# Kernel tuning notes

Measured on AMD Instinct MI355X. Metric: run time of the kernel, lower is better.

The kernel has to match this reference:

```python
import jax, jax.numpy as jnp
import numpy as np

S, N, L = 64, 256, 32
LANG_ID, D = 256, 128  # lang_od == pc_od == D
K = 16  # k; effective neighbors = k+1


def _mlp(x, w1, b1, w2, b2):
    return jnp.maximum(x @ w1 + b1, 0.0) @ w2 + b2


def setup_inputs() -> dict:
    key = jax.random.key(0)
    ks = jax.random.split(key, 16)
    def lin(k, fi, fo):
        return jax.random.normal(k, (fi, fo), jnp.float32) / np.sqrt(fi)
    inp = {
        "feat": jax.random.normal(ks[0], (S, N, D), jnp.float32),
        "coord": jax.random.normal(ks[1], (S, N, 3), jnp.float32),
        "lang_feat": jax.random.normal(ks[2], (S, L, LANG_ID), jnp.float32),
        "lang_len": jax.random.randint(ks[3], (S,), 1, L + 1),
        "rel_w1": lin(ks[4], 10, D), "rel_b1": jnp.zeros((D,), jnp.float32),
        "rel_w2": lin(ks[5], D, D), "rel_b2": jnp.zeros((D,), jnp.float32),
        "lang_w1": lin(ks[6], LANG_ID, D), "lang_b1": jnp.zeros((D,), jnp.float32),
        "lang_w2": lin(ks[7], D, D), "lang_b2": jnp.zeros((D,), jnp.float32),
        "feat_w1": lin(ks[8], D, D), "feat_b1": jnp.zeros((D,), jnp.float32),
        "feat_w2": lin(ks[9], D, D), "feat_b2": jnp.zeros((D,), jnp.float32),
    }
    return inp


def reference(feat, coord, lang_feat, lang_len,
              rel_w1, rel_b1, rel_w2, rel_b2,
              lang_w1, lang_b1, lang_w2, lang_b2,
              feat_w1, feat_b1, feat_w2, feat_b2):
    num_sen, num_obj, _ = feat.shape
    k1 = min(K, num_obj - 1) + 1  # k+1 neighbors including self
    # pairwise squared distances [S,N,N]
    d = ((coord[:, None, :, :] - coord[:, :, None, :]) ** 2).sum(-1)
    # k+1 nearest neighbors (smallest distance)
    _, idx = jax.lax.top_k(-d, k1)  # [S,N,k1]
    b = jnp.arange(num_sen)[:, None, None]
    coord_nb = coord[b, idx]  # [S,N,k1,3]
    coord_ctr = jnp.broadcast_to(coord[:, :, None, :], coord_nb.shape)
    rel_coord = coord_nb - coord_ctr
    dist = jnp.sqrt((rel_coord ** 2).sum(-1, keepdims=True))
    rel = jnp.concatenate([coord_nb, coord_ctr, rel_coord, dist], -1)  # [S,N,k1,10]
    rel = _mlp(rel, rel_w1, rel_b1, rel_w2, rel_b2)  # [S,N,k1,D]
    lang = _mlp(lang_feat, lang_w1, lang_b1, lang_w2, lang_b2)  # [S,L,D]
    f = _mlp(feat, feat_w1, feat_b1, feat_w2, feat_b2)  # [S,N,D]
    f_nb = f[b, idx]  # [S,N,k1,D]
    # attention of each (obj, neighbor) over language tokens
    attn = jnp.einsum('snkd,sld->snkl', f_nb, lang)
    attn = jax.nn.softmax(attn, axis=-1)
    max_len = lang_feat.shape[1]
    mask = (jnp.arange(max_len)[None, :] < lang_len[:, None]).astype(f.dtype)  # [S,L]
    attn = attn * mask[:, None, None, :]
    attn = attn / (attn.sum(-1, keepdims=True) + 1e-7)
    ins = jnp.einsum('snkl,sld->snkd', attn, lang)  # [S,N,k1,D]
    out = (f_nb * ins * rel).sum(2) + f  # [S,N,D]
    score = out.sum(-1)  # [S,N]
    return out, score
```

## Files before the change

### kernel.cpp

```cpp
#include <hip/hip_runtime.h>
#include <math.h>

#define S_ 64
#define N_ 256
#define L_ 32
#define D_ 128
#define LID_ 256
#define K1_ 17
#define CH_ 32
#define NW_ 8

typedef __attribute__((ext_vector_type(8))) short short8;
typedef __attribute__((ext_vector_type(4))) float f32x4;

__device__ __forceinline__ unsigned short f2bf(float f) {
  unsigned int u = __float_as_uint(f);
  u += 0x7fffu + ((u >> 16) & 1u);
  return (unsigned short)(u >> 16);
}


__global__ __launch_bounds__(256) void tar_prep_kernel(
    const float* __restrict__ rw1, const float* __restrict__ rb1,
    const float* __restrict__ rw2, const float* __restrict__ fw1,
    const float* __restrict__ fw2, unsigned short* __restrict__ w1T,
    unsigned short* __restrict__ w2T, unsigned short* __restrict__ fw1T,
    unsigned short* __restrict__ fw2T) {
  int t = blockIdx.x * 256 + threadIdx.x;
  int k = t >> 7, n = t & 127;
  int slot = 32 * (k >> 5) + 8 * ((k & 15) >> 2) + 4 * ((k >> 4) & 1) + (k & 3);
  w2T[(size_t)n * 128 + slot] = f2bf(rw2[(size_t)k * 128 + n]);
  fw1T[(size_t)n * 128 + k] = f2bf(fw1[(size_t)k * 128 + n]);
  fw2T[(size_t)n * 128 + k] = f2bf(fw2[(size_t)k * 128 + n]);
  if (t < 128 * 16) {
    int n2 = t >> 4, k2 = t & 15;
    unsigned short v = 0;
    if (k2 < 10) v = f2bf(rw1[(size_t)k2 * 128 + n2]);
    else if (k2 == 10) v = f2bf(rb1[n2]);
    w1T[(size_t)n2 * 16 + k2] = v;
  }
}

#define KNN_NB 1024
#define LANG_NB 1024
#define FM_NB 256
__global__ __launch_bounds__(256, 4) void tar_prologue(
    const float* __restrict__ coord, int* __restrict__ idx_out,
    const float* __restrict__ lx, const float* __restrict__ lw1,
    const float* __restrict__ lb1, const float* __restrict__ lw2,
    const float* __restrict__ lb2, unsigned short* __restrict__ lang_bf,
    unsigned short* __restrict__ langT_bf, const float* __restrict__ fx,
    const unsigned short* __restrict__ fw1T, const float* __restrict__ fb1,
    const unsigned short* __restrict__ fw2T, const float* __restrict__ fb2,
    float* __restrict__ f_out, unsigned short* __restrict__ f_bf) {
  __shared__ __align__(16) char uarena[34816];
  int bid = blockIdx.x;
  int tid = threadIdx.x;

  if (bid < KNN_NB) {
    int wv = tid >> 6, l = tid & 63, grp = l >> 4, ln16 = l & 15;
    int obj = bid * 16 + wv * 4 + grp;
    int s = obj >> 8, n = obj & 255;
    const float* cs = coord + (size_t)s * N_ * 3;
    float cx = cs[n * 3 + 0], cy = cs[n * 3 + 1], cz = cs[n * 3 + 2];
    unsigned kd[16];
#pragma unroll
    for (int q = 0; q < 16; ++q) {
      int j = ln16 + q * 16;
      float dx = cs[j * 3 + 0] - cx;
      float dy = cs[j * 3 + 1] - cy;
      float dz = cs[j * 3 + 2] - cz;
      kd[q] = __float_as_uint(dx * dx + dy * dy + dz * dz);
    }
    for (int k = 0; k < K1_; ++k) {
      unsigned m = kd[0];
#pragma unroll
      for (int q = 1; q < 16; ++q) m = min(m, kd[q]);
      int bq = 0;
#pragma unroll
      for (int q = 15; q >= 0; --q)
        if (kd[q] == m) bq = q;
      int bj = ln16 + bq * 16;
      unsigned bm = m;
#pragma unroll
      for (int off = 1; off <= 8; off <<= 1) {
        unsigned om = __shfl_xor(bm, off);
        int oj = __shfl_xor(bj, off);
        if (om < bm || (om == bm && oj < bj)) { bm = om; bj = oj; }
      }
#pragma unroll
      for (int q = 0; q < 16; ++q)
        if (ln16 + q * 16 == bj) kd[q] = 0xFFFFFFFFu;
      if (ln16 == 0) idx_out[(size_t)obj * K1_ + k] = bj;
    }
  } else if (bid < KNN_NB + LANG_NB) {
    float* sx = (float*)uarena;
    float* sh = (float*)(uarena + 2048);
    int sub = tid >> 7, j = tid & 127;
    int row = (bid - KNN_NB) * 2 + sub;
    const float* xr = lx + (size_t)row * LID_;
    sx[sub * 256 + j] = xr[j];
    sx[sub * 256 + j + 128] = xr[j + 128];
    __syncthreads();
    float acc = lb1[j];
#pragma unroll 8
    for (int i = 0; i < LID_; ++i) acc += sx[sub * 256 + i] * lw1[i * D_ + j];
    sh[sub * 128 + j] = fmaxf(acc, 0.f);
    __syncthreads();
    float acc2 = lb2[j];
#pragma unroll 8
    for (int hh = 0; hh < D_; ++hh) acc2 += sh[sub * 128 + hh] * lw2[hh * D_ + j];
    unsigned short hb = f2bf(acc2);
    lang_bf[(size_t)row * D_ + j] = hb;
    int s = row >> 5, t = row & 31;
    int slot = 8 * ((t & 15) >> 2) + 4 * (t >> 4) + (t & 3);
    langT_bf[((size_t)s * D_ + j) * L_ + slot] = hb;
  } else {
    unsigned short* x_s = (unsigned short*)uarena;
    unsigned short* h_s = (unsigned short*)(uarena + 17408);
    int base = (bid - KNN_NB - LANG_NB) * 64;
    int w = tid >> 6, l = tid & 63, g = l >> 4, ln = l & 15;
    for (int i = tid; i < 64 * 32; i += 256) {
      int row = i >> 5, c4 = (i & 31) * 4;
      float4 v = *(const float4*)&fx[(size_t)(base + row) * D_ + c4];
      unsigned short* dst = &x_s[row * 136 + c4];
      dst[0] = f2bf(v.x); dst[1] = f2bf(v.y);
      dst[2] = f2bf(v.z); dst[3] = f2bf(v.w);
    }
    __syncthreads();
    float b1v[8], b2v[8];
#pragma unroll
    for (int nt = 0; nt < 8; ++nt) {
      b1v[nt] = fb1[nt * 16 + ln];
      b2v[nt] = fb2[nt * 16 + ln];
    }
    short8 a1[4];
#pragma unroll
    for (int kk = 0; kk < 4; ++kk)
      a1[kk] = *(const short8*)&x_s[(w * 16 + ln) * 136 + kk * 32 + g * 8];
    unsigned short* hw = &h_s[w * 16 * 136];
#pragma unroll
    for (int nt = 0; nt < 8; ++nt) {
      f32x4 acc = {b1v[nt], b1v[nt], b1v[nt], b1v[nt]};
#pragma unroll
      for (int kk = 0; kk < 4; ++kk) {
        short8 bw =
            *(const short8*)&fw1T[(size_t)(nt * 16 + ln) * 128 + kk * 32 + g * 8];
        acc = __builtin_amdgcn_mfma_f32_16x16x32_bf16(a1[kk], bw, acc, 0, 0, 0);
      }
#pragma unroll
      for (int reg = 0; reg < 4; ++reg)
        hw[(g * 4 + reg) * 136 + nt * 16 + ln] = f2bf(fmaxf(acc[reg], 0.f));
    }
    short8 a2[4];
#pragma unroll
    for (int kk = 0; kk < 4; ++kk)
      a2[kk] = *(const short8*)&hw[ln * 136 + kk * 32 + g * 8];
#pragma unroll
    for (int nt = 0; nt < 8; ++nt) {
      f32x4 acc = {b2v[nt], b2v[nt], b2v[nt], b2v[nt]};
#pragma unroll
      for (int kk = 0; kk < 4; ++kk) {
        short8 bw =
            *(const short8*)&fw2T[(size_t)(nt * 16 + ln) * 128 + kk * 32 + g * 8];
        acc = __builtin_amdgcn_mfma_f32_16x16x32_bf16(a2[kk], bw, acc, 0, 0, 0);
      }
#pragma unroll
      for (int reg = 0; reg < 4; ++reg) {
        int row = base + w * 16 + g * 4 + reg;
        int col = nt * 16 + ln;
        f_out[(size_t)row * D_ + col] = acc[reg];
        f_bf[(size_t)row * D_ + col] = f2bf(acc[reg]);
      }
    }
  }
}

__global__ __launch_bounds__(512, 2) void tar_main_mfma(
    const float* __restrict__ f_out, const unsigned short* __restrict__ f_bf,
    const unsigned short* __restrict__ lang_bf,
    const unsigned short* __restrict__ langT_bf, const int* __restrict__ idxg,
    const float* __restrict__ coord, const unsigned short* __restrict__ w1T_bf,
    const unsigned short* __restrict__ w2T_bf, const float* __restrict__ rel_b2,
    const int* __restrict__ lang_len, float* __restrict__ outp,
    float* __restrict__ score) {
  __shared__ __align__(16) char arena[40960];
  __shared__ float score_s[CH_];

  unsigned short* lang_s = (unsigned short*)(arena);
  unsigned short* langT_s = (unsigned short*)(arena + 8704);
  unsigned short* w1T_s = (unsigned short*)(arena + 18944);
  int* idx_s = (int*)(arena + 25088);

  int b = blockIdx.x;
  int s = b >> 3;
  int chunk = b & 7;
  int sn0 = s * N_ + chunk * CH_;
  int tid = threadIdx.x;
  int w = tid >> 6;
  int l = tid & 63;
  int g = l >> 4;
  int ln = l & 15;
  int og = w >> 2;
  int h = (w >> 1) & 1;
  int q2 = w & 1;
  int len = lang_len[s];

  {
    int row = tid >> 4, c0 = (tid & 15) * 8;
    *(short8*)&lang_s[row * 136 + c0] =
        *(const short8*)&lang_bf[((size_t)s * L_ + row) * D_ + c0];
  }
  {
    int row = tid >> 2, c0 = (tid & 3) * 8;
    *(short8*)&langT_s[row * 40 + c0] =
        *(const short8*)&langT_bf[((size_t)s * D_ + row) * L_ + c0];
  }
  if (tid < 256) {
    int row = tid >> 1, c0 = (tid & 1) * 8;
    *(short8*)&w1T_s[row * 24 + c0] =
        *(const short8*)&w1T_bf[(size_t)row * 16 + c0];
  }
  for (int i = tid; i < CH_ * K1_; i += 512)
    idx_s[i] = idxg[(size_t)sn0 * K1_ + i];
  if (tid < CH_) score_s[tid] = 0.f;
  __syncthreads();

  float b2v[4];
#pragma unroll
  for (int j = 0; j < 4; ++j) b2v[j] = rel_b2[(h * 4 + j) * 16 + ln];

  f32x4 o[4];
#pragma unroll
  for (int j = 0; j < 4; ++j) o[j] = (f32x4){0.f, 0.f, 0.f, 0.f};

  int objA = og * 16 + ln;
  const float* fbase = &f_out[(size_t)s * N_ * D_];
  const float* cA = coord + (size_t)(sn0 + objA) * 3;
  float cx = cA[0], cy = cA[1], cz = cA[2];

  for (int k = q2; k < K1_; k += 2) {
    int nbrA = idx_s[objA * K1_ + k];
    int nbrC[4];
#pragma unroll
    for (int reg = 0; reg < 4; ++reg)
      nbrC[reg] = idx_s[(og * 16 + g * 4 + reg) * K1_ + k];

    const float* cN = coord + (size_t)(s * N_ + nbrA) * 3;
    float nx = cN[0], ny = cN[1], nz = cN[2];
    float rx = nx - cx, ry = ny - cy, rz = nz - cz;
    float dist = sqrtf(rx * rx + ry * ry + rz * rz);
    short8 a1v = {0, 0, 0, 0, 0, 0, 0, 0};
    if (g == 0) {
      a1v[0] = (short)f2bf(nx); a1v[1] = (short)f2bf(ny);
      a1v[2] = (short)f2bf(nz); a1v[3] = (short)f2bf(cx);
      a1v[4] = (short)f2bf(cy); a1v[5] = (short)f2bf(cz);
      a1v[6] = (short)f2bf(rx); a1v[7] = (short)f2bf(ry);
    } else if (g == 1) {
      a1v[0] = (short)f2bf(rz);
      a1v[1] = (short)f2bf(dist);
      a1v[2] = (short)0x3F80;
    }

    const unsigned short* fArow = &f_bf[((size_t)s * N_ + nbrA) * D_];

    f32x4 at0 = {0.f, 0.f, 0.f, 0.f}, at1 = {0.f, 0.f, 0.f, 0.f};
#pragma unroll
    for (int kk = 0; kk < 4; ++kk) {
      short8 fA = *(const short8*)&fArow[kk * 32 + g * 8];
      short8 bb0 = *(const short8*)&lang_s[ln * 136 + kk * 32 + g * 8];
      short8 bb1 = *(const short8*)&lang_s[(16 + ln) * 136 + kk * 32 + g * 8];
      at0 = __builtin_amdgcn_mfma_f32_16x16x32_bf16(bb0, fA, at0, 0, 0, 0);
      at1 = __builtin_amdgcn_mfma_f32_16x16x32_bf16(bb1, fA, at1, 0, 0, 0);
    }

    float mx = fmaxf(fmaxf(fmaxf(at0[0], at0[1]), fmaxf(at0[2], at0[3])),
                     fmaxf(fmaxf(at1[0], at1[1]), fmaxf(at1[2], at1[3])));
    mx = fmaxf(mx, __shfl_xor(mx, 16));
    mx = fmaxf(mx, __shfl_xor(mx, 32));
    float e0[4], e1[4], p0[4], p1[4];
    float ss = 0.f, ms = 0.f;
#pragma unroll
    for (int reg = 0; reg < 4; ++reg) {
      e0[reg] = expf(at0[reg] - mx);
      e1[reg] = expf(at1[reg] - mx);
      ss += e0[reg] + e1[reg];
      p0[reg] = (4 * g + reg < len) ? e0[reg] : 0.f;
      p1[reg] = (16 + 4 * g + reg < len) ? e1[reg] : 0.f;
      ms += p0[reg] + p1[reg];
    }
    ss += __shfl_xor(ss, 16);
    ss += __shfl_xor(ss, 32);
    ms += __shfl_xor(ms, 16);
    ms += __shfl_xor(ms, 32);
    float inv = 1.0f / (ms + 1e-7f * ss);
    short8 pa;
#pragma unroll
    for (int reg = 0; reg < 4; ++reg) {
      pa[reg] = (short)f2bf(p0[reg] * inv);
      pa[4 + reg] = (short)f2bf(p1[reg] * inv);
    }

    short8 a2[4];
#pragma unroll
    for (int kk = 0; kk < 4; ++kk) {
      short8 bw0 = {0, 0, 0, 0, 0, 0, 0, 0};
      short8 bw1 = {0, 0, 0, 0, 0, 0, 0, 0};
      if (g < 2) {
        bw0 = *(const short8*)&w1T_s[((2 * kk) * 16 + ln) * 24 + g * 8];
        bw1 = *(const short8*)&w1T_s[((2 * kk + 1) * 16 + ln) * 24 + g * 8];
      }
      f32x4 z = {0.f, 0.f, 0.f, 0.f};
      f32x4 r0 = __builtin_amdgcn_mfma_f32_16x16x32_bf16(bw0, a1v, z, 0, 0, 0);
      f32x4 r1 = __builtin_amdgcn_mfma_f32_16x16x32_bf16(bw1, a1v, z, 0, 0, 0);
#pragma unroll
      for (int reg = 0; reg < 4; ++reg) {
        a2[kk][reg] = (short)f2bf(fmaxf(r0[reg], 0.f));
        a2[kk][4 + reg] = (short)f2bf(fmaxf(r1[reg], 0.f));
      }
    }

#pragma unroll
    for (int j = 0; j < 4; ++j) {
      int nt = h * 4 + j;
      f32x4 ro = {b2v[j], b2v[j], b2v[j], b2v[j]};
#pragma unroll
      for (int kk = 0; kk < 4; ++kk) {
        short8 bw =
            *(const short8*)&w2T_bf[(size_t)(nt * 16 + ln) * 128 + kk * 32 + g * 8];
        ro = __builtin_amdgcn_mfma_f32_16x16x32_bf16(a2[kk], bw, ro, 0, 0, 0);
      }
      f32x4 iv = {0.f, 0.f, 0.f, 0.f};
      short8 bl = *(const short8*)&langT_s[(nt * 16 + ln) * 40 + g * 8];
      iv = __builtin_amdgcn_mfma_f32_16x16x32_bf16(pa, bl, iv, 0, 0, 0);
#pragma unroll
      for (int reg = 0; reg < 4; ++reg) {
        float fv = fbase[(size_t)nbrC[reg] * D_ + nt * 16 + ln];
        o[j][reg] += fv * iv[reg] * ro[reg];
      }
    }
  }

  __syncthreads();
  float* R = (float*)arena;
  {
    float* Rw = R + w * 1280;
#pragma unroll
    for (int j = 0; j < 4; ++j)
      *(f32x4*)&Rw[(j * 16 + ln) * 20 + g * 4] = o[j];
  }
  __syncthreads();
  {
    int wp = og * 4 + h * 2;
    float vs[2][4];
#pragma unroll
    for (int t = 0; t < 2; ++t) {
      int j = q2 * 2 + t;
      int col = (h * 4 + j) * 16 + ln;
      f32x4 sum = *(f32x4*)&R[wp * 1280 + (j * 16 + ln) * 20 + g * 4];
      sum += *(f32x4*)&R[(wp + 1) * 1280 + (j * 16 + ln) * 20 + g * 4];
#pragma unroll
      for (int reg = 0; reg < 4; ++reg) {
        int obj = og * 16 + g * 4 + reg;
        float v = sum[reg] + f_out[(size_t)(sn0 + obj) * D_ + col];
        outp[(size_t)(sn0 + obj) * D_ + col] = v;
        vs[t][reg] = v;
      }
    }
#pragma unroll
    for (int reg = 0; reg < 4; ++reg) {
      float sv = vs[0][reg] + vs[1][reg];
      sv += __shfl_xor(sv, 1);
      sv += __shfl_xor(sv, 2);
      sv += __shfl_xor(sv, 4);
      sv += __shfl_xor(sv, 8);
      if (ln == 0) atomicAdd(&score_s[og * 16 + g * 4 + reg], sv);
    }
  }
  __syncthreads();
  if (tid < CH_) score[sn0 + tid] = score_s[tid];
}

extern "C" void kernel_launch(void* const* d_in, const int* in_sizes, int n_in,
                              void* d_out, int out_size, void* d_ws,
                              size_t ws_size, hipStream_t stream) {
  const float* feat = (const float*)d_in[0];
  const float* coord = (const float*)d_in[1];
  const float* lang_feat = (const float*)d_in[2];
  const int* lang_len = (const int*)d_in[3];
  const float* rel_w1 = (const float*)d_in[4];
  const float* rel_b1 = (const float*)d_in[5];
  const float* rel_w2 = (const float*)d_in[6];
  const float* rel_b2 = (const float*)d_in[7];
  const float* lang_w1 = (const float*)d_in[8];
  const float* lang_b1 = (const float*)d_in[9];
  const float* lang_w2 = (const float*)d_in[10];
  const float* lang_b2 = (const float*)d_in[11];
  const float* feat_w1 = (const float*)d_in[12];
  const float* feat_b1 = (const float*)d_in[13];
  const float* feat_w2 = (const float*)d_in[14];
  const float* feat_b2 = (const float*)d_in[15];

  char* ws = (char*)d_ws;
  unsigned short* lang_bf = (unsigned short*)(ws);
  unsigned short* langT_bf = (unsigned short*)(ws + 524288);
  float* f_out = (float*)(ws + 1048576);
  unsigned short* f_bf = (unsigned short*)(ws + 9437184);
  int* idx = (int*)(ws + 13631488);
  unsigned short* w2T_bf = (unsigned short*)(ws + 14745600);
  unsigned short* w1T_bf = (unsigned short*)(ws + 14778368);
  unsigned short* fw1T_bf = (unsigned short*)(ws + 14782464);
  unsigned short* fw2T_bf = (unsigned short*)(ws + 14815232);

  float* out = (float*)d_out;
  float* score = out + (size_t)S_ * N_ * D_;

  tar_prep_kernel<<<dim3(64), dim3(256), 0, stream>>>(
      rel_w1, rel_b1, rel_w2, feat_w1, feat_w2, w1T_bf, w2T_bf, fw1T_bf,
      fw2T_bf);
  tar_prologue<<<dim3(KNN_NB + LANG_NB + FM_NB), dim3(256), 0, stream>>>(
      coord, idx, lang_feat, lang_w1, lang_b1, lang_w2, lang_b2, lang_bf,
      langT_bf, feat, fw1T_bf, feat_b1, fw2T_bf, feat_b2, f_out, f_bf);
  tar_main_mfma<<<dim3(S_ * (N_ / CH_)), dim3(512), 0, stream>>>(
      f_out, f_bf, lang_bf, langT_bf, idx, coord, w1T_bf, w2T_bf, rel_b2,
      lang_len, out, score);
}
```

Measured before the change: 119.8 us.

## Move language MLP to bf16 MFMA, stage rel W2 in LDS, use packed bf16 converts

The language MLP blocks are rewritten from scalar fp32 dot products, one row per half block, into bf16 MFMA tiles of 64 rows per block, fed by new transposed bf16 copies of the language weights. The main kernel now stages the relation MLP's second weight matrix in shared memory instead of reading it from global memory for every tile. It also replaces scalar bf16 rounding with the packed v_cvt_pk_bf16_f32 instruction in several places. The larger LDS footprint in the main and prologue kernels may lower occupancy, and bf16 for the language MLP changes numerics.

```diff
diff --git a/kernel.cpp b/kernel.cpp
--- a/kernel.cpp
+++ b/kernel.cpp
@@ -18,21 +18,37 @@
   u += 0x7fffu + ((u >> 16) & 1u);
   return (unsigned short)(u >> 16);
 }
+__device__ __forceinline__ unsigned cvt_pk_bf16(float a, float b) {
+  unsigned r;
+  asm("v_cvt_pk_bf16_f32 %0, %1, %2" : "=v"(r) : "v"(a), "v"(b));
+  return r;
+}
+union U8 { short8 s8; unsigned u[4]; };
 
 
 __global__ __launch_bounds__(256) void tar_prep_kernel(
     const float* __restrict__ rw1, const float* __restrict__ rb1,
     const float* __restrict__ rw2, const float* __restrict__ fw1,
-    const float* __restrict__ fw2, unsigned short* __restrict__ w1T,
+    const float* __restrict__ fw2, const float* __restrict__ lw1,
+    const float* __restrict__ lw2, unsigned short* __restrict__ w1T,
     unsigned short* __restrict__ w2T, unsigned short* __restrict__ fw1T,
-    unsigned short* __restrict__ fw2T) {
+    unsigned short* __restrict__ fw2T, unsigned short* __restrict__ lw1T,
+    unsigned short* __restrict__ lw2T) {
   int t = blockIdx.x * 256 + threadIdx.x;
-  int k = t >> 7, n = t & 127;
-  int slot = 32 * (k >> 5) + 8 * ((k & 15) >> 2) + 4 * ((k >> 4) & 1) + (k & 3);
-  w2T[(size_t)n * 128 + slot] = f2bf(rw2[(size_t)k * 128 + n]);
-  fw1T[(size_t)n * 128 + k] = f2bf(fw1[(size_t)k * 128 + n]);
-  fw2T[(size_t)n * 128 + k] = f2bf(fw2[(size_t)k * 128 + n]);
-  if (t < 128 * 16) {
+  {
+    int k = t >> 7, n = t & 127;
+    lw1T[(size_t)n * 256 + k] = f2bf(lw1[(size_t)k * 128 + n]);
+  }
+  if (t < 16384) {
+    int k = t >> 7, n = t & 127;
+    int slot =
+        32 * (k >> 5) + 8 * ((k & 15) >> 2) + 4 * ((k >> 4) & 1) + (k & 3);
+    w2T[(size_t)n * 128 + slot] = f2bf(rw2[(size_t)k * 128 + n]);
+    fw1T[(size_t)n * 128 + k] = f2bf(fw1[(size_t)k * 128 + n]);
+    fw2T[(size_t)n * 128 + k] = f2bf(fw2[(size_t)k * 128 + n]);
+    lw2T[(size_t)n * 128 + k] = f2bf(lw2[(size_t)k * 128 + n]);
+  }
+  if (t < 2048) {
     int n2 = t >> 4, k2 = t & 15;
     unsigned short v = 0;
     if (k2 < 10) v = f2bf(rw1[(size_t)k2 * 128 + n2]);
@@ -42,18 +58,18 @@
 }
 
 #define KNN_NB 1024
-#define LANG_NB 1024
+#define LANG_NB 32
 #define FM_NB 256
 __global__ __launch_bounds__(256, 4) void tar_prologue(
     const float* __restrict__ coord, int* __restrict__ idx_out,
-    const float* __restrict__ lx, const float* __restrict__ lw1,
-    const float* __restrict__ lb1, const float* __restrict__ lw2,
+    const float* __restrict__ lx, const unsigned short* __restrict__ lw1T,
+    const float* __restrict__ lb1, const unsigned short* __restrict__ lw2T,
     const float* __restrict__ lb2, unsigned short* __restrict__ lang_bf,
     unsigned short* __restrict__ langT_bf, const float* __restrict__ fx,
     const unsigned short* __restrict__ fw1T, const float* __restrict__ fb1,
     const unsigned short* __restrict__ fw2T, const float* __restrict__ fb2,
     float* __restrict__ f_out, unsigned short* __restrict__ f_bf) {
-  __shared__ __align__(16) char uarena[34816];
+  __shared__ __align__(16) char uarena[51200];
   int bid = blockIdx.x;
   int tid = threadIdx.x;
 
@@ -94,27 +110,67 @@
       if (ln16 == 0) idx_out[(size_t)obj * K1_ + k] = bj;
     }
   } else if (bid < KNN_NB + LANG_NB) {
-    float* sx = (float*)uarena;
-    float* sh = (float*)(uarena + 2048);
-    int sub = tid >> 7, j = tid & 127;
-    int row = (bid - KNN_NB) * 2 + sub;
-    const float* xr = lx + (size_t)row * LID_;
-    sx[sub * 256 + j] = xr[j];
-    sx[sub * 256 + j + 128] = xr[j + 128];
+    unsigned short* x_s = (unsigned short*)uarena;
+    unsigned short* h_s = (unsigned short*)(uarena + 33792);
+    int base = (bid - KNN_NB) * 64;
+    int w = tid >> 6, l = tid & 63, g = l >> 4, ln = l & 15;
+    for (int i = tid; i < 64 * 64; i += 256) {
+      int row = i >> 6, c4 = (i & 63) * 4;
+      float4 v = *(const float4*)&lx[(size_t)(base + row) * LID_ + c4];
+      uint2 uv;
+      uv.x = cvt_pk_bf16(v.x, v.y);
+      uv.y = cvt_pk_bf16(v.z, v.w);
+      *(uint2*)&x_s[row * 264 + c4] = uv;
+    }
     __syncthreads();
-    float acc = lb1[j];
-#pragma unroll 8
-    for (int i = 0; i < LID_; ++i) acc += sx[sub * 256 + i] * lw1[i * D_ + j];
-    sh[sub * 128 + j] = fmaxf(acc, 0.f);
-    __syncthreads();
-    float acc2 = lb2[j];
-#pragma unroll 8
-    for (int hh = 0; hh < D_; ++hh) acc2 += sh[sub * 128 + hh] * lw2[hh * D_ + j];
-    unsigned short hb = f2bf(acc2);
-    lang_bf[(size_t)row * D_ + j] = hb;
-    int s = row >> 5, t = row & 31;
-    int slot = 8 * ((t & 15) >> 2) + 4 * (t >> 4) + (t & 3);
-    langT_bf[((size_t)s * D_ + j) * L_ + slot] = hb;
+    float b1v[8], b2v[8];
+#pragma unroll
+    for (int nt = 0; nt < 8; ++nt) {
+      b1v[nt] = lb1[nt * 16 + ln];
+      b2v[nt] = lb2[nt * 16 + ln];
+    }
+    short8 a1[8];
+#pragma unroll
+    for (int kk = 0; kk < 8; ++kk)
+      a1[kk] = *(const short8*)&x_s[(w * 16 + ln) * 264 + kk * 32 + g * 8];
+    unsigned short* hw = &h_s[w * 16 * 136];
+#pragma unroll
+    for (int nt = 0; nt < 8; ++nt) {
+      f32x4 acc = {b1v[nt], b1v[nt], b1v[nt], b1v[nt]};
+#pragma unroll
+      for (int kk = 0; kk < 8; ++kk) {
+        short8 bw =
+            *(const short8*)&lw1T[(size_t)(nt * 16 + ln) * 256 + kk * 32 + g * 8];
+        acc = __builtin_amdgcn_mfma_f32_16x16x32_bf16(a1[kk], bw, acc, 0, 0, 0);
+      }
+#pragma unroll
+      for (int reg = 0; reg < 4; ++reg)
+        hw[(g * 4 + reg) * 136 + nt * 16 + ln] = f2bf(fmaxf(acc[reg], 0.f));
+    }
+    short8 a2[4];
+#pragma unroll
+    for (int kk = 0; kk < 4; ++kk)
+      a2[kk] = *(const short8*)&hw[ln * 136 + kk * 32 + g * 8];
+#pragma unroll
+    for (int nt = 0; nt < 8; ++nt) {
+      f32x4 acc = {b2v[nt], b2v[nt], b2v[nt], b2v[nt]};
+#pragma unroll
+      for (int kk = 0; kk < 4; ++kk) {
+        short8 bw =
+            *(const short8*)&lw2T[(size_t)(nt * 16 + ln) * 128 + kk * 32 + g * 8];
+        acc = __builtin_amdgcn_mfma_f32_16x16x32_bf16(a2[kk], bw, acc, 0, 0, 0);
+      }
+#pragma unroll
+      for (int reg = 0; reg < 4; ++reg) {
+        int row = base + w * 16 + g * 4 + reg;
+        int col = nt * 16 + ln;
+        unsigned short hb = f2bf(acc[reg]);
+        lang_bf[(size_t)row * D_ + col] = hb;
+        int s = row >> 5, t = row & 31;
+        int slot = 8 * ((t & 15) >> 2) + 4 * (t >> 4) + (t & 3);
+        langT_bf[((size_t)s * D_ + col) * L_ + slot] = hb;
+      }
+    }
   } else {
     unsigned short* x_s = (unsigned short*)uarena;
     unsigned short* h_s = (unsigned short*)(uarena + 17408);
@@ -123,9 +179,10 @@
     for (int i = tid; i < 64 * 32; i += 256) {
       int row = i >> 5, c4 = (i & 31) * 4;
       float4 v = *(const float4*)&fx[(size_t)(base + row) * D_ + c4];
-      unsigned short* dst = &x_s[row * 136 + c4];
-      dst[0] = f2bf(v.x); dst[1] = f2bf(v.y);
-      dst[2] = f2bf(v.z); dst[3] = f2bf(v.w);
+      uint2 uv;
+      uv.x = cvt_pk_bf16(v.x, v.y);
+      uv.y = cvt_pk_bf16(v.z, v.w);
+      *(uint2*)&x_s[row * 136 + c4] = uv;
     }
     __syncthreads();
     float b1v[8], b2v[8];
@@ -184,13 +241,14 @@
     const unsigned short* __restrict__ w2T_bf, const float* __restrict__ rel_b2,
     const int* __restrict__ lang_len, float* __restrict__ outp,
     float* __restrict__ score) {
-  __shared__ __align__(16) char arena[40960];
+  __shared__ __align__(16) char arena[62080];
   __shared__ float score_s[CH_];
 
   unsigned short* lang_s = (unsigned short*)(arena);
   unsigned short* langT_s = (unsigned short*)(arena + 8704);
   unsigned short* w1T_s = (unsigned short*)(arena + 18944);
   int* idx_s = (int*)(arena + 25088);
+  unsigned short* w2T_s = (unsigned short*)(arena + 27264);
 
   int b = blockIdx.x;
   int s = b >> 3;
@@ -220,6 +278,11 @@
     int row = tid >> 1, c0 = (tid & 1) * 8;
     *(short8*)&w1T_s[row * 24 + c0] =
         *(const short8*)&w1T_bf[(size_t)row * 16 + c0];
+  }
+  for (int i = tid; i < 2048; i += 512) {
+    int row = i >> 4, c0 = (i & 15) * 8;
+    *(short8*)&w2T_s[row * 136 + c0] =
+        *(const short8*)&w2T_bf[(size_t)row * 128 + c0];
   }
   for (int i = tid; i < CH_ * K1_; i += 512)
     idx_s[i] = idxg[(size_t)sn0 * K1_ + i];
@@ -294,12 +357,12 @@
     ms += __shfl_xor(ms, 16);
     ms += __shfl_xor(ms, 32);
     float inv = 1.0f / (ms + 1e-7f * ss);
-    short8 pa;
-#pragma unroll
-    for (int reg = 0; reg < 4; ++reg) {
-      pa[reg] = (short)f2bf(p0[reg] * inv);
-      pa[4 + reg] = (short)f2bf(p1[reg] * inv);
-    }
+    U8 pau;
+    pau.u[0] = cvt_pk_bf16(p0[0] * inv, p0[1] * inv);
+    pau.u[1] = cvt_pk_bf16(p0[2] * inv, p0[3] * inv);
+    pau.u[2] = cvt_pk_bf16(p1[0] * inv, p1[1] * inv);
+    pau.u[3] = cvt_pk_bf16(p1[2] * inv, p1[3] * inv);
+    short8 pa = pau.s8;
 
     short8 a2[4];
 #pragma unroll
@@ -313,11 +376,12 @@
       f32x4 z = {0.f, 0.f, 0.f, 0.f};
       f32x4 r0 = __builtin_amdgcn_mfma_f32_16x16x32_bf16(bw0, a1v, z, 0, 0, 0);
       f32x4 r1 = __builtin_amdgcn_mfma_f32_16x16x32_bf16(bw1, a1v, z, 0, 0, 0);
-#pragma unroll
-      for (int reg = 0; reg < 4; ++reg) {
-        a2[kk][reg] = (short)f2bf(fmaxf(r0[reg], 0.f));
-        a2[kk][4 + reg] = (short)f2bf(fmaxf(r1[reg], 0.f));
-      }
+      U8 au;
+      au.u[0] = cvt_pk_bf16(fmaxf(r0[0], 0.f), fmaxf(r0[1], 0.f));
+      au.u[1] = cvt_pk_bf16(fmaxf(r0[2], 0.f), fmaxf(r0[3], 0.f));
+      au.u[2] = cvt_pk_bf16(fmaxf(r1[0], 0.f), fmaxf(r1[1], 0.f));
+      au.u[3] = cvt_pk_bf16(fmaxf(r1[2], 0.f), fmaxf(r1[3], 0.f));
+      a2[kk] = au.s8;
     }
 
 #pragma unroll
@@ -327,7 +391,7 @@
 #pragma unroll
       for (int kk = 0; kk < 4; ++kk) {
         short8 bw =
-            *(const short8*)&w2T_bf[(size_t)(nt * 16 + ln) * 128 + kk * 32 + g * 8];
+            *(const short8*)&w2T_s[(nt * 16 + ln) * 136 + kk * 32 + g * 8];
         ro = __builtin_amdgcn_mfma_f32_16x16x32_bf16(a2[kk], bw, ro, 0, 0, 0);
       }
       f32x4 iv = {0.f, 0.f, 0.f, 0.f};
@@ -411,15 +475,17 @@
   unsigned short* w1T_bf = (unsigned short*)(ws + 14778368);
   unsigned short* fw1T_bf = (unsigned short*)(ws + 14782464);
   unsigned short* fw2T_bf = (unsigned short*)(ws + 14815232);
+  unsigned short* lw1T_bf = (unsigned short*)(ws + 14848000);
+  unsigned short* lw2T_bf = (unsigned short*)(ws + 14913536);
 
   float* out = (float*)d_out;
   float* score = out + (size_t)S_ * N_ * D_;
 
-  tar_prep_kernel<<<dim3(64), dim3(256), 0, stream>>>(
-      rel_w1, rel_b1, rel_w2, feat_w1, feat_w2, w1T_bf, w2T_bf, fw1T_bf,
-      fw2T_bf);
+  tar_prep_kernel<<<dim3(128), dim3(256), 0, stream>>>(
+      rel_w1, rel_b1, rel_w2, feat_w1, feat_w2, lang_w1, lang_w2, w1T_bf,
+      w2T_bf, fw1T_bf, fw2T_bf, lw1T_bf, lw2T_bf);
   tar_prologue<<<dim3(KNN_NB + LANG_NB + FM_NB), dim3(256), 0, stream>>>(
-      coord, idx, lang_feat, lang_w1, lang_b1, lang_w2, lang_b2, lang_bf,
+      coord, idx, lang_feat, lw1T_bf, lang_b1, lw2T_bf, lang_b2, lang_bf,
       langT_bf, feat, fw1T_bf, feat_b1, fw2T_bf, feat_b2, f_out, f_bf);
   tar_main_mfma<<<dim3(S_ * (N_ / CH_)), dim3(512), 0, stream>>>(
       f_out, f_bf, lang_bf, langT_bf, idx, coord, w1T_bf, w2T_bf, rel_b2,
```

After: 139.7 us. 1.17x slower.
